# Performance work log

Measured on AMD Instinct MI355X. Metric: run time of the kernel, lower is better.

The kernel has to match this reference:

```python
import jax, jax.numpy as jnp
import numpy as np

B, T, I, H = 256, 256, 512, 1024


def setup_inputs() -> dict:
    key = jax.random.key(0)
    ks = jax.random.split(key, 16)
    sx = 1.0 / np.sqrt(I)
    sh = 1.0 / np.sqrt(H)
    d = {
        "x": jax.random.normal(ks[0], (B, T, I), jnp.float32),
        "Wfx": jax.random.normal(ks[1], (H, I), jnp.float32) * sx,
        "Wfh": jax.random.normal(ks[2], (H, H), jnp.float32) * sh,
        "bf": jnp.zeros((H,), jnp.float32),
        "Wix": jax.random.normal(ks[3], (H, I), jnp.float32) * sx,
        "Wih": jax.random.normal(ks[4], (H, H), jnp.float32) * sh,
        "bi": jnp.zeros((H,), jnp.float32),
        "Wox": jax.random.normal(ks[5], (H, I), jnp.float32) * sx,
        "Woh": jax.random.normal(ks[6], (H, H), jnp.float32) * sh,
        "bo": jnp.zeros((H,), jnp.float32),
        "Wcx": jax.random.normal(ks[7], (H, I), jnp.float32) * sx,
        "Wch": jax.random.normal(ks[8], (H, H), jnp.float32) * sh,
        "bc": jnp.zeros((H,), jnp.float32),
        "W1": jax.random.normal(ks[9], (64, H), jnp.float32) * sh,
        "b1": jnp.zeros((64,), jnp.float32),
        "W2": jax.random.normal(ks[10], (10, 64), jnp.float32) * (1.0 / 8.0),
        "b2": jnp.zeros((10,), jnp.float32),
    }
    return d


def reference(x, Wfx, Wfh, bf, Wix, Wih, bi, Wox, Woh, bo, Wcx, Wch, bc, W1, b1, W2, b2):
    b, t, _ = x.shape
    h0 = jnp.zeros((b, Wfh.shape[0]), x.dtype)
    c0 = jnp.zeros_like(h0)

    def step(carry, xt):  # xt: [B, I]
        h, c = carry
        f = jax.nn.sigmoid(xt @ Wfx.T + h @ Wfh.T + bf)
        i = jax.nn.sigmoid(xt @ Wix.T + h @ Wih.T + bi)
        o = jax.nn.sigmoid(xt @ Wox.T + h @ Woh.T + bo)
        ct = jnp.tanh(xt @ Wcx.T + h @ Wch.T + bc)
        c = f * c + i * ct
        h = o * jnp.tanh(c)
        return (h, c), None

    (h, c), _ = jax.lax.scan(step, (h0, c0), jnp.swapaxes(x, 0, 1))
    h = jax.nn.relu(h)
    h1 = jax.nn.relu(h @ W1.T + b1)
    logits = h1 @ W2.T + b2
    return jax.nn.softmax(logits, axis=1)
```

## Files before the change

kernel.cpp:

```cpp
#include <hip/hip_runtime.h>

#define BB 256
#define TT 256
#define II 512
#define HH 1024

typedef _Float16 h16;
typedef __attribute__((ext_vector_type(4))) _Float16 h16x4;
typedef __attribute__((ext_vector_type(8))) _Float16 h16x8;
typedef __attribute__((ext_vector_type(4))) float f32x4;
typedef __attribute__((ext_vector_type(4))) unsigned int u32x4;

#define KPADH 1032
#define ABUF_BYTES 66048
#define PRE_OFF 66048
#define SMEM_BYTES 99840

#define WX_OFF   0UL
#define WH_OFF   4194304UL
#define BIAS_OFF 12582912UL
#define W1T_OFF  12599296UL
#define HBUF_OFF 12861440UL
#define ARR_OFF  13910016UL
#define XH_OFF   13914112UL
#define XH_END   81022976UL

#define HSTRIDE (BB * HH)

__device__ __forceinline__ float sigm(float x) { return 1.0f / (1.0f + __expf(-x)); }
__device__ __forceinline__ float tanh_(float x) { float e = __expf(2.0f * x); return 1.0f - 2.0f / (e + 1.0f); }

__global__ void k_prep(const float* __restrict__ Wfx, const float* __restrict__ Wfh, const float* __restrict__ bf,
                       const float* __restrict__ Wix, const float* __restrict__ Wih, const float* __restrict__ bi,
                       const float* __restrict__ Wox, const float* __restrict__ Woh, const float* __restrict__ bo,
                       const float* __restrict__ Wcx, const float* __restrict__ Wch, const float* __restrict__ bc,
                       const float* __restrict__ W1,
                       h16* __restrict__ Wx, h16* __restrict__ Wh, float* __restrict__ bias, float* __restrict__ W1T)
{
  const long NWX = 4096L * 512, NWH = 4096L * 1024, NB = 4096, NW1 = 1024L * 64;
  const long total = NWX + NWH + NB + NW1;
  for (long id = blockIdx.x * 256L + threadIdx.x; id < total; id += gridDim.x * 256L) {
    if (id < NWX) {
      long n = id >> 9, k = id & 511;
      long g = n >> 10, j = n & 1023;
      const float* s = (g == 0) ? Wfx : (g == 1) ? Wix : (g == 2) ? Wox : Wcx;
      Wx[id] = (h16)s[j * II + k];
    } else if (id < NWX + NWH) {
      long i2 = id - NWX;
      long n = i2 >> 10, k = i2 & 1023;
      long g = n >> 10, j = n & 1023;
      const float* s = (g == 0) ? Wfh : (g == 1) ? Wih : (g == 2) ? Woh : Wch;
      Wh[i2] = (h16)s[j * HH + k];
    } else if (id < NWX + NWH + NB) {
      long n = id - NWX - NWH;
      long g = n >> 10, j = n & 1023;
      const float* s = (g == 0) ? bf : (g == 1) ? bi : (g == 2) ? bo : bc;
      bias[n] = s[j];
    } else {
      long i2 = id - NWX - NWH - NB;
      long k = i2 >> 6, n = i2 & 63;
      W1T[i2] = W1[n * HH + k];
    }
  }
}

__global__ void k_castx(const float* __restrict__ x, h16* __restrict__ xh) {
  const long n = (long)BB * TT * II;
  for (long i = (blockIdx.x * 256L + threadIdx.x) * 4; i < n; i += gridDim.x * 1024L) {
    float4 v = *(const float4*)(x + i);
    h16x4 o = {(h16)v.x, (h16)v.y, (h16)v.z, (h16)v.w};
    *(h16x4*)(xh + i) = o;
  }
}

template <int USE_XH>
__global__ __launch_bounds__(512, 1) void k_lstm(
    const float* __restrict__ x32, const h16* __restrict__ x16,
    const h16* __restrict__ Wx, const h16* __restrict__ Wh,
    const float* __restrict__ bias,
    h16* __restrict__ hbuf, unsigned int* __restrict__ arr)
{
  extern __shared__ char smem[];
  h16* Abuf = (h16*)smem;
  float* Pre = (float*)(smem + PRE_OFF);

  const int tid = threadIdx.x;
  const int wid = tid >> 6;
  const int lane = tid & 63;
  const int lm = lane & 15;
  const int lq = lane >> 4;

  const int bx = blockIdx.x;
  const int group = bx >> 5;
  const int nslice = bx & 31;
  const int r0 = group * 32;
  const int hc0 = nslice * 32;

  const int g = wid >> 1;
  const int kh = wid & 1;

  const int ng0 = g * HH + hc0 + lm;
  const int ng1 = ng0 + 16;
  const float bs0 = (kh == 0) ? bias[ng0] : 0.f;
  const float bs1 = (kh == 0) ? bias[ng1] : 0.f;

  const h16* WxB0 = Wx + (size_t)ng0 * II + kh * 256 + lq * 8;
  const h16* WxB1 = Wx + (size_t)ng1 * II + kh * 256 + lq * 8;

  h16x8 wh0[16], wh1[16];
  {
    const h16* p0 = Wh + (size_t)ng0 * HH + kh * 512 + lq * 8;
    const h16* p1 = Wh + (size_t)ng1 * HH + kh * 512 + lq * 8;
#pragma unroll
    for (int kk = 0; kk < 16; ++kk) {
      wh0[kk] = *(const h16x8*)(p0 + kk * 32);
      wh1[kk] = *(const h16x8*)(p1 + kk * 32);
    }
  }

  const size_t TI = (size_t)TT * II;
  const float* xr32_0 = x32 + (size_t)(r0 + lm) * TI + kh * 256 + lq * 8;
  const float* xr32_1 = xr32_0 + 16 * TI;
  const h16* xr16_0 = x16 + (size_t)(r0 + lm) * TI + kh * 256 + lq * 8;
  const h16* xr16_1 = xr16_0 + 16 * TI;

  const int aB0 = lm * KPADH + kh * 512 + lq * 8;
  const int aB1 = (16 + lm) * KPADH + kh * 512 + lq * 8;

  const int urow = tid >> 4;
  const int ucolp = (tid & 15) * 2;
  float cst[2] = {0.f, 0.f};

  unsigned int* slots = arr + group * 32;
  unsigned int* myslot = slots + nslice;

  for (int t = 0; t < TT; ++t) {
    f32x4 a00 = {bs0, bs0, bs0, bs0};
    f32x4 a01 = {bs1, bs1, bs1, bs1};
    f32x4 a10 = a00;
    f32x4 a11 = a01;

    u32x4 stg[8];
    if (t > 0) {
      if (tid < 32) {
        const unsigned int* sp = slots + tid;
        unsigned int v;
        do {
          asm volatile("global_load_dword %0, %1, off sc0 sc1\n\t"
                       "s_waitcnt vmcnt(0)"
                       : "=v"(v) : "v"(sp) : "memory");
        } while (__any(v < (unsigned int)t));
      }
      __syncthreads();
      {
        const h16* hs = hbuf + (size_t)((t - 1) & 1) * HSTRIDE + (size_t)r0 * HH;
#pragma unroll
        for (int j = 0; j < 8; ++j) {
          int c = tid + j * 512;
          const h16* p = hs + (size_t)(c >> 7) * HH + (c & 127) * 8;
          asm volatile("global_load_dwordx4 %0, %1, off sc0 sc1"
                       : "=v"(stg[j]) : "v"(p) : "memory");
        }
      }
    }

#pragma unroll 2
    for (int kk = 0; kk < 8; ++kk) {
      h16x8 xa0, xa1;
      if (USE_XH) {
        xa0 = *(const h16x8*)(xr16_0 + (size_t)t * II + kk * 32);
        xa1 = *(const h16x8*)(xr16_1 + (size_t)t * II + kk * 32);
      } else {
        const float* p0 = xr32_0 + (size_t)t * II + kk * 32;
        const float* p1 = xr32_1 + (size_t)t * II + kk * 32;
        float4 u0 = *(const float4*)(p0), v0 = *(const float4*)(p0 + 4);
        float4 u1 = *(const float4*)(p1), v1 = *(const float4*)(p1 + 4);
        xa0 = (h16x8){(h16)u0.x, (h16)u0.y, (h16)u0.z, (h16)u0.w, (h16)v0.x, (h16)v0.y, (h16)v0.z, (h16)v0.w};
        xa1 = (h16x8){(h16)u1.x, (h16)u1.y, (h16)u1.z, (h16)u1.w, (h16)v1.x, (h16)v1.y, (h16)v1.z, (h16)v1.w};
      }
      h16x8 xb0 = *(const h16x8*)(WxB0 + kk * 32);
      h16x8 xb1 = *(const h16x8*)(WxB1 + kk * 32);
      a00 = __builtin_amdgcn_mfma_f32_16x16x32_f16(xa0, xb0, a00, 0, 0, 0);
      a01 = __builtin_amdgcn_mfma_f32_16x16x32_f16(xa0, xb1, a01, 0, 0, 0);
      a10 = __builtin_amdgcn_mfma_f32_16x16x32_f16(xa1, xb0, a10, 0, 0, 0);
      a11 = __builtin_amdgcn_mfma_f32_16x16x32_f16(xa1, xb1, a11, 0, 0, 0);
    }

    if (t > 0) {
      asm volatile("s_waitcnt vmcnt(0)" ::: "memory");
#pragma unroll
      for (int j = 0; j < 8; ++j) {
        int c = tid + j * 512;
        *(u32x4*)(Abuf + (c >> 7) * KPADH + (c & 127) * 8) = stg[j];
      }
      __syncthreads();
#pragma unroll
      for (int kk = 0; kk < 16; ++kk) {
        h16x8 ha0 = *(const h16x8*)(Abuf + aB0 + kk * 32);
        h16x8 ha1 = *(const h16x8*)(Abuf + aB1 + kk * 32);
        a00 = __builtin_amdgcn_mfma_f32_16x16x32_f16(ha0, wh0[kk], a00, 0, 0, 0);
        a01 = __builtin_amdgcn_mfma_f32_16x16x32_f16(ha0, wh1[kk], a01, 0, 0, 0);
        a10 = __builtin_amdgcn_mfma_f32_16x16x32_f16(ha1, wh0[kk], a10, 0, 0, 0);
        a11 = __builtin_amdgcn_mfma_f32_16x16x32_f16(ha1, wh1[kk], a11, 0, 0, 0);
      }
    }

    {
      float* Pg = Pre + (size_t)(g * 2 + kh) * 32 * 33;
#pragma unroll
      for (int i = 0; i < 4; ++i) {
        int rA = lq * 4 + i;
        Pg[rA * 33 + lm]              = a00[i];
        Pg[rA * 33 + 16 + lm]         = a01[i];
        Pg[(16 + rA) * 33 + lm]       = a10[i];
        Pg[(16 + rA) * 33 + 16 + lm]  = a11[i];
      }
    }
    __syncthreads();
    {
      float hv[2];
#pragma unroll
      for (int cc = 0; cc < 2; ++cc) {
        int col = ucolp + cc;
        float fp = Pre[(0 * 32 + urow) * 33 + col] + Pre[(1 * 32 + urow) * 33 + col];
        float ip = Pre[(2 * 32 + urow) * 33 + col] + Pre[(3 * 32 + urow) * 33 + col];
        float op = Pre[(4 * 32 + urow) * 33 + col] + Pre[(5 * 32 + urow) * 33 + col];
        float cp = Pre[(6 * 32 + urow) * 33 + col] + Pre[(7 * 32 + urow) * 33 + col];
        float c2 = sigm(fp) * cst[cc] + sigm(ip) * tanh_(cp);
        cst[cc] = c2;
        hv[cc] = sigm(op) * tanh_(c2);
      }
      union { h16 h[2]; unsigned int u; } pk;
      pk.h[0] = (h16)hv[0]; pk.h[1] = (h16)hv[1];
      const h16* hp = hbuf + (size_t)(t & 1) * HSTRIDE + (size_t)(r0 + urow) * HH + hc0 + ucolp;
      asm volatile("global_store_dword %0, %1, off sc0 sc1"
                   :: "v"(hp), "v"(pk.u) : "memory");
    }
    __builtin_amdgcn_s_waitcnt(0);
    __syncthreads();
    if (tid == 0) {
      unsigned int val = (unsigned int)(t + 1);
      asm volatile("global_store_dword %0, %1, off sc0 sc1"
                   :: "v"(myslot), "v"(val) : "memory");
    }
  }
}

__global__ void k_head(const h16* __restrict__ hbuf, const float* __restrict__ W1T,
                       const float* __restrict__ b1, const float* __restrict__ W2,
                       const float* __restrict__ b2, float* __restrict__ out)
{
  __shared__ float hrow[1024];
  __shared__ float part[64][5];
  __shared__ float h1[64];
  __shared__ float logit[10];
  int r = blockIdx.x, tid = threadIdx.x;
  for (int i = tid; i < 1024; i += 256) {
    float v = (float)hbuf[(size_t)r * HH + i];
    hrow[i] = v > 0.f ? v : 0.f;
  }
  __syncthreads();
  int n = tid & 63, q = tid >> 6;
  float s = 0.f;
  for (int i = 0; i < 256; ++i) s += hrow[q * 256 + i] * W1T[(q * 256 + i) * 64 + n];
  part[n][q] = s;
  __syncthreads();
  if (tid < 64) {
    float v = part[tid][0] + part[tid][1] + part[tid][2] + part[tid][3] + b1[tid];
    h1[tid] = v > 0.f ? v : 0.f;
  }
  __syncthreads();
  if (tid < 10) {
    float s2 = b2[tid];
    for (int k = 0; k < 64; ++k) s2 += h1[k] * W2[tid * 64 + k];
    logit[tid] = s2;
  }
  __syncthreads();
  if (tid < 10) {
    float m = logit[0];
    for (int i = 1; i < 10; ++i) m = fmaxf(m, logit[i]);
    float sum = 0.f;
    for (int i = 0; i < 10; ++i) sum += __expf(logit[i] - m);
    out[r * 10 + tid] = __expf(logit[tid] - m) / sum;
  }
}

extern "C" void kernel_launch(void* const* d_in, const int* in_sizes, int n_in,
                              void* d_out, int out_size, void* d_ws, size_t ws_size,
                              hipStream_t stream) {
  const float* x   = (const float*)d_in[0];
  const float* Wfx = (const float*)d_in[1];
  const float* Wfh = (const float*)d_in[2];
  const float* bf  = (const float*)d_in[3];
  const float* Wix = (const float*)d_in[4];
  const float* Wih = (const float*)d_in[5];
  const float* bi  = (const float*)d_in[6];
  const float* Wox = (const float*)d_in[7];
  const float* Woh = (const float*)d_in[8];
  const float* bo  = (const float*)d_in[9];
  const float* Wcx = (const float*)d_in[10];
  const float* Wch = (const float*)d_in[11];
  const float* bc  = (const float*)d_in[12];
  const float* W1  = (const float*)d_in[13];
  const float* b1  = (const float*)d_in[14];
  const float* W2  = (const float*)d_in[15];
  const float* b2  = (const float*)d_in[16];
  (void)in_sizes; (void)n_in; (void)out_size;

  char* ws = (char*)d_ws;
  h16* Wx = (h16*)(ws + WX_OFF);
  h16* Wh = (h16*)(ws + WH_OFF);
  float* bias = (float*)(ws + BIAS_OFF);
  float* W1T = (float*)(ws + W1T_OFF);
  h16* hbuf = (h16*)(ws + HBUF_OFF);
  unsigned int* arr = (unsigned int*)(ws + ARR_OFF);
  h16* xh = (h16*)(ws + XH_OFF);
  const int use_xh = (ws_size >= XH_END) ? 1 : 0;

  hipMemsetAsync(arr, 0, 4096, stream);
  k_prep<<<4096, 256, 0, stream>>>(Wfx, Wfh, bf, Wix, Wih, bi, Wox, Woh, bo, Wcx, Wch, bc, W1,
                                   Wx, Wh, bias, W1T);
  if (use_xh) k_castx<<<8192, 256, 0, stream>>>(x, xh);

  (void)hipFuncSetAttribute(reinterpret_cast<const void*>(&k_lstm<1>),
                            hipFuncAttributeMaxDynamicSharedMemorySize, SMEM_BYTES);
  (void)hipFuncSetAttribute(reinterpret_cast<const void*>(&k_lstm<0>),
                            hipFuncAttributeMaxDynamicSharedMemorySize, SMEM_BYTES);
  if (use_xh)
    k_lstm<1><<<256, 512, SMEM_BYTES, stream>>>(x, xh, Wx, Wh, bias, hbuf, arr);
  else
    k_lstm<0><<<256, 512, SMEM_BYTES, stream>>>(x, xh, Wx, Wh, bias, hbuf, arr);

  k_head<<<256, 256, 0, stream>>>(hbuf + HSTRIDE, W1T, b1, W2, b2, (float*)d_out);
}
```

Before: 3.192 ms.

## Use per-wave arrival flags and overlap input projection with barrier wait

Replaces the per-block arrival counter with per-wave 16-bit flags. Every wave now polls all 256 flags of its group directly, which removes the block-wide __syncthreads both before loading h and after storing it. Half of the x-projection MFMAs are moved ahead of the poll so they overlap the wait for other blocks. The Pre scratch stride is padded to 34 so the gate values can be read as float2. The cost is more polling traffic per wave, and correctness now depends on every wave publishing its own flag.

```diff
diff --git a/kernel.cpp b/kernel.cpp
--- a/kernel.cpp
+++ b/kernel.cpp
@@ -9,12 +9,14 @@
 typedef __attribute__((ext_vector_type(4))) _Float16 h16x4;
 typedef __attribute__((ext_vector_type(8))) _Float16 h16x8;
 typedef __attribute__((ext_vector_type(4))) float f32x4;
+typedef __attribute__((ext_vector_type(2))) unsigned int u32x2;
 typedef __attribute__((ext_vector_type(4))) unsigned int u32x4;
 
 #define KPADH 1032
-#define ABUF_BYTES 66048
 #define PRE_OFF 66048
-#define SMEM_BYTES 99840
+#define PRESTRIDE 34
+#define PRESLAB (32 * PRESTRIDE)
+#define SMEM_BYTES 100864
 
 #define WX_OFF   0UL
 #define WH_OFF   4194304UL
@@ -78,7 +80,7 @@
     const float* __restrict__ x32, const h16* __restrict__ x16,
     const h16* __restrict__ Wx, const h16* __restrict__ Wh,
     const float* __restrict__ bias,
-    h16* __restrict__ hbuf, unsigned int* __restrict__ arr)
+    h16* __restrict__ hbuf, unsigned short* __restrict__ arr)
 {
   extern __shared__ char smem[];
   h16* Abuf = (h16*)smem;
@@ -131,8 +133,9 @@
   const int ucolp = (tid & 15) * 2;
   float cst[2] = {0.f, 0.f};
 
-  unsigned int* slots = arr + group * 32;
-  unsigned int* myslot = slots + nslice;
+  unsigned short* slots = arr + group * 256;
+  unsigned short* myslot = slots + nslice * 8 + wid;
+  const unsigned short* pollp = slots + lane * 4;
 
   for (int t = 0; t < TT; ++t) {
     f32x4 a00 = {bs0, bs0, bs0, bs0};
@@ -140,18 +143,44 @@
     f32x4 a10 = a00;
     f32x4 a11 = a01;
 
+    const size_t tOff = (size_t)t * II;
+
+#pragma unroll
+    for (int kk = 0; kk < 4; ++kk) {
+      h16x8 xa0, xa1;
+      if (USE_XH) {
+        xa0 = *(const h16x8*)(xr16_0 + tOff + kk * 32);
+        xa1 = *(const h16x8*)(xr16_1 + tOff + kk * 32);
+      } else {
+        const float* p0 = xr32_0 + tOff + kk * 32;
+        const float* p1 = xr32_1 + tOff + kk * 32;
+        float4 u0 = *(const float4*)(p0), v0 = *(const float4*)(p0 + 4);
+        float4 u1 = *(const float4*)(p1), v1 = *(const float4*)(p1 + 4);
+        xa0 = (h16x8){(h16)u0.x, (h16)u0.y, (h16)u0.z, (h16)u0.w, (h16)v0.x, (h16)v0.y, (h16)v0.z, (h16)v0.w};
+        xa1 = (h16x8){(h16)u1.x, (h16)u1.y, (h16)u1.z, (h16)u1.w, (h16)v1.x, (h16)v1.y, (h16)v1.z, (h16)v1.w};
+      }
+      h16x8 xb0 = *(const h16x8*)(WxB0 + kk * 32);
+      h16x8 xb1 = *(const h16x8*)(WxB1 + kk * 32);
+      a00 = __builtin_amdgcn_mfma_f32_16x16x32_f16(xa0, xb0, a00, 0, 0, 0);
+      a01 = __builtin_amdgcn_mfma_f32_16x16x32_f16(xa0, xb1, a01, 0, 0, 0);
+      a10 = __builtin_amdgcn_mfma_f32_16x16x32_f16(xa1, xb0, a10, 0, 0, 0);
+      a11 = __builtin_amdgcn_mfma_f32_16x16x32_f16(xa1, xb1, a11, 0, 0, 0);
+    }
+
     u32x4 stg[8];
     if (t > 0) {
-      if (tid < 32) {
-        const unsigned int* sp = slots + tid;
-        unsigned int v;
+      {
+        u32x2 vv;
+        unsigned int mn;
         do {
-          asm volatile("global_load_dword %0, %1, off sc0 sc1\n\t"
+          asm volatile("global_load_dwordx2 %0, %1, off sc0 sc1\n\t"
                        "s_waitcnt vmcnt(0)"
-                       : "=v"(v) : "v"(sp) : "memory");
-        } while (__any(v < (unsigned int)t));
-      }
-      __syncthreads();
+                       : "=v"(vv) : "v"(pollp) : "memory");
+          unsigned int m0 = vv.x & 0xffffu, m1 = vv.x >> 16;
+          unsigned int m2 = vv.y & 0xffffu, m3 = vv.y >> 16;
+          mn = min(min(m0, m1), min(m2, m3));
+        } while (__any(mn < (unsigned int)t));
+      }
       {
         const h16* hs = hbuf + (size_t)((t - 1) & 1) * HSTRIDE + (size_t)r0 * HH;
 #pragma unroll
@@ -164,15 +193,15 @@
       }
     }
 
-#pragma unroll 2
-    for (int kk = 0; kk < 8; ++kk) {
+#pragma unroll
+    for (int kk = 4; kk < 8; ++kk) {
       h16x8 xa0, xa1;
       if (USE_XH) {
-        xa0 = *(const h16x8*)(xr16_0 + (size_t)t * II + kk * 32);
-        xa1 = *(const h16x8*)(xr16_1 + (size_t)t * II + kk * 32);
+        xa0 = *(const h16x8*)(xr16_0 + tOff + kk * 32);
+        xa1 = *(const h16x8*)(xr16_1 + tOff + kk * 32);
       } else {
-        const float* p0 = xr32_0 + (size_t)t * II + kk * 32;
-        const float* p1 = xr32_1 + (size_t)t * II + kk * 32;
+        const float* p0 = xr32_0 + tOff + kk * 32;
+        const float* p1 = xr32_1 + tOff + kk * 32;
         float4 u0 = *(const float4*)(p0), v0 = *(const float4*)(p0 + 4);
         float4 u1 = *(const float4*)(p1), v1 = *(const float4*)(p1 + 4);
         xa0 = (h16x8){(h16)u0.x, (h16)u0.y, (h16)u0.z, (h16)u0.w, (h16)v0.x, (h16)v0.y, (h16)v0.z, (h16)v0.w};
@@ -206,29 +235,39 @@
     }
 
     {
-      float* Pg = Pre + (size_t)(g * 2 + kh) * 32 * 33;
+      float* Pg = Pre + (size_t)(g * 2 + kh) * PRESLAB;
 #pragma unroll
       for (int i = 0; i < 4; ++i) {
         int rA = lq * 4 + i;
-        Pg[rA * 33 + lm]              = a00[i];
-        Pg[rA * 33 + 16 + lm]         = a01[i];
-        Pg[(16 + rA) * 33 + lm]       = a10[i];
-        Pg[(16 + rA) * 33 + 16 + lm]  = a11[i];
+        Pg[rA * PRESTRIDE + lm]              = a00[i];
+        Pg[rA * PRESTRIDE + 16 + lm]         = a01[i];
+        Pg[(16 + rA) * PRESTRIDE + lm]       = a10[i];
+        Pg[(16 + rA) * PRESTRIDE + 16 + lm]  = a11[i];
       }
     }
     __syncthreads();
     {
+      const float* Pq = Pre + urow * PRESTRIDE + ucolp;
+      float2 q0 = *(const float2*)(Pq + 0 * PRESLAB);
+      float2 q1 = *(const float2*)(Pq + 1 * PRESLAB);
+      float2 q2 = *(const float2*)(Pq + 2 * PRESLAB);
+      float2 q3 = *(const float2*)(Pq + 3 * PRESLAB);
+      float2 q4 = *(const float2*)(Pq + 4 * PRESLAB);
+      float2 q5 = *(const float2*)(Pq + 5 * PRESLAB);
+      float2 q6 = *(const float2*)(Pq + 6 * PRESLAB);
+      float2 q7 = *(const float2*)(Pq + 7 * PRESLAB);
       float hv[2];
-#pragma unroll
-      for (int cc = 0; cc < 2; ++cc) {
-        int col = ucolp + cc;
-        float fp = Pre[(0 * 32 + urow) * 33 + col] + Pre[(1 * 32 + urow) * 33 + col];
-        float ip = Pre[(2 * 32 + urow) * 33 + col] + Pre[(3 * 32 + urow) * 33 + col];
-        float op = Pre[(4 * 32 + urow) * 33 + col] + Pre[(5 * 32 + urow) * 33 + col];
-        float cp = Pre[(6 * 32 + urow) * 33 + col] + Pre[(7 * 32 + urow) * 33 + col];
-        float c2 = sigm(fp) * cst[cc] + sigm(ip) * tanh_(cp);
-        cst[cc] = c2;
-        hv[cc] = sigm(op) * tanh_(c2);
+      {
+        float fp = q0.x + q1.x, ip = q2.x + q3.x, op = q4.x + q5.x, cp = q6.x + q7.x;
+        float c2 = sigm(fp) * cst[0] + sigm(ip) * tanh_(cp);
+        cst[0] = c2;
+        hv[0] = sigm(op) * tanh_(c2);
+      }
+      {
+        float fp = q0.y + q1.y, ip = q2.y + q3.y, op = q4.y + q5.y, cp = q6.y + q7.y;
+        float c2 = sigm(fp) * cst[1] + sigm(ip) * tanh_(cp);
+        cst[1] = c2;
+        hv[1] = sigm(op) * tanh_(c2);
       }
       union { h16 h[2]; unsigned int u; } pk;
       pk.h[0] = (h16)hv[0]; pk.h[1] = (h16)hv[1];
@@ -236,11 +275,10 @@
       asm volatile("global_store_dword %0, %1, off sc0 sc1"
                    :: "v"(hp), "v"(pk.u) : "memory");
     }
-    __builtin_amdgcn_s_waitcnt(0);
-    __syncthreads();
-    if (tid == 0) {
+    asm volatile("s_waitcnt vmcnt(0)" ::: "memory");
+    if (lane == 0) {
       unsigned int val = (unsigned int)(t + 1);
-      asm volatile("global_store_dword %0, %1, off sc0 sc1"
+      asm volatile("global_store_short %0, %1, off sc0 sc1"
                    :: "v"(myslot), "v"(val) : "memory");
     }
   }
@@ -313,7 +351,7 @@
   float* bias = (float*)(ws + BIAS_OFF);
   float* W1T = (float*)(ws + W1T_OFF);
   h16* hbuf = (h16*)(ws + HBUF_OFF);
-  unsigned int* arr = (unsigned int*)(ws + ARR_OFF);
+  unsigned short* arr = (unsigned short*)(ws + ARR_OFF);
   h16* xh = (h16*)(ws + XH_OFF);
   const int use_xh = (ws_size >= XH_END) ? 1 : 0;
 
```

After: 2.872 ms, median of 2. 1.11x faster.
